# Kernel tuning notes

Measured on AMD Instinct MI355X. Metric: run time of the kernel, lower is better.

The kernel has to match this reference:

```python
import jax, jax.numpy as jnp
import numpy as np

N_NODES = 100000
N_REL = 8
F_IN, F_HID, F_OUT = 64, 64, 32
N_EDGES = 1000000


def rgcn_conv(x, W, root, bias, src, dst, edge_type):
    """PyG RGCNConv with default aggr='mean': out[i] = sum_r mean_{j in N_r(i)} W_r x_j + root x_i + bias."""
    R, _, O = W.shape
    N = x.shape[0]
    # Transform every node under every relation: [R, N, O]
    h = jnp.einsum('nf,rfo->rno', x, W)
    # Gather per-edge messages: [E, O]
    msg = h[edge_type, src]
    # Per-(relation, dst) mean aggregation via combined segment ids
    seg = edge_type * N + dst
    sums = jax.ops.segment_sum(msg, seg, num_segments=R * N).reshape(R, N, O)
    cnt = jax.ops.segment_sum(jnp.ones((msg.shape[0],), msg.dtype), seg,
                              num_segments=R * N).reshape(R, N, 1)
    mean = sums / jnp.maximum(cnt, 1.0)  # empty neighborhoods -> 0
    return mean.sum(axis=0) + x @ root + bias


def setup_inputs() -> dict:
    key = jax.random.key(0)
    ks = jax.random.split(key, 9)
    s = lambda fan: 1.0 / np.sqrt(fan)
    x = jax.random.normal(ks[0], (N_NODES, F_IN), jnp.float32)
    edge_index = jax.random.randint(ks[1], (2, N_EDGES), 0, N_NODES, jnp.int64)
    edge_type = jax.random.randint(ks[2], (N_EDGES,), 0, N_REL, jnp.int64)
    W1 = jax.random.normal(ks[3], (N_REL, F_IN, F_HID), jnp.float32) * s(F_IN)
    root1 = jax.random.normal(ks[4], (F_IN, F_HID), jnp.float32) * s(F_IN)
    b1 = jnp.zeros((F_HID,), jnp.float32)
    W2 = jax.random.normal(ks[5], (N_REL, F_HID, F_OUT), jnp.float32) * s(F_HID)
    root2 = jax.random.normal(ks[6], (F_HID, F_OUT), jnp.float32) * s(F_HID)
    b2 = jnp.zeros((F_OUT,), jnp.float32)
    return {"x": x, "W1": W1, "root1": root1, "b1": b1,
            "W2": W2, "root2": root2, "b2": b2,
            "edge_index": edge_index, "edge_type": edge_type}


def reference(x, W1, root1, b1, W2, root2, b2, edge_index, edge_type):
    src, dst = edge_index[0], edge_index[1]
    # encode (dropout is identity in eval mode)
    h = jax.nn.relu(rgcn_conv(x, W1, root1, b1, src, dst, edge_type))
    z = rgcn_conv(h, W2, root2, b2, src, dst, edge_type)
    # decode: gather-dot-product link scores over the same edge list
    return (z[src] * z[dst]).sum(axis=1)
```

## Files before the change

### kernel.cpp

```cpp
#include <hip/hip_runtime.h>

#define F_IN 64
#define F_HID 64
#define F_OUT 32
#define NREL 8
#define SCAP 6144
#define MAXBUCK 200
#define PA_PE 16

typedef __attribute__((ext_vector_type(8))) short bfrag;
typedef __attribute__((ext_vector_type(4))) float ffrag;

__device__ inline unsigned short f2bf(float f) {
  unsigned u = __float_as_uint(f);
  unsigned r = (u + 0x7fffu + ((u >> 16) & 1u)) >> 16;
  return (unsigned short)r;
}
__device__ inline unsigned bf16pair(float lo, float hi) {
  return (unsigned)f2bf(lo) | ((unsigned)f2bf(hi) << 16);
}
__device__ inline float bflo(unsigned u) { return __uint_as_float(u << 16); }
__device__ inline float bfhi(unsigned u) { return __uint_as_float(u & 0xffff0000u); }
__device__ inline float dot8(uint4 a, uint4 b) {
  return bflo(a.x) * bflo(b.x) + bfhi(a.x) * bfhi(b.x) +
         bflo(a.y) * bflo(b.y) + bfhi(a.y) * bfhi(b.y) +
         bflo(a.z) * bflo(b.z) + bfhi(a.z) * bfhi(b.z) +
         bflo(a.w) * bflo(b.w) + bfhi(a.w) * bfhi(b.w);
}

template <int O, bool PERMK>
__device__ inline void wprep_one(int t, const float* __restrict__ W,
                                 const float* __restrict__ root,
                                 unsigned short* __restrict__ Wf) {
  constexpr int CT = O / 16;
  int l = t & 63;
  int s = (t >> 6) & 1;
  int rc = t >> 7;
  int c = rc % CT;
  int r = rc / CT;
  const float* wsrc = (r < NREL) ? W + (size_t)r * 64 * O : root;
  unsigned short* dst = Wf + (size_t)t * 8;
  int col = c * 16 + (l & 15);
  int k0 = s * 32 + ((l >> 4) * 8);
#pragma unroll
  for (int j = 0; j < 8; ++j) {
    int k = k0 + j;
    if (PERMK) k = (k & 3) * 16 + (k >> 2);
    dst[j] = f2bf(wsrc[(size_t)k * O + col]);
  }
}

__global__ __launch_bounds__(256) void prep_kernel(
    const float* __restrict__ W1, const float* __restrict__ root1,
    const float* __restrict__ W2, const float* __restrict__ root2,
    unsigned short* __restrict__ wf1, unsigned short* __restrict__ wf2,
    int* __restrict__ gcur, int nbuck) {
  int gid = blockIdx.x * 256 + threadIdx.x;
  const int J1 = (NREL + 1) * (F_HID / 16) * 2 * 64;
  const int J2 = (NREL + 1) * (F_OUT / 16) * 2 * 64;
  if (gid < J1) {
    wprep_one<F_HID, false>(gid, W1, root1, wf1);
  } else if (gid < J1 + J2) {
    wprep_one<F_OUT, true>(gid - J1, W2, root2, wf2);
  } else if (gid - J1 - J2 < nbuck) {
    int b = gid - J1 - J2;
    gcur[b] = b * SCAP;
  }
}

__global__ __launch_bounds__(256) void cvt_bf16_kernel(
    const float* __restrict__ in, unsigned* __restrict__ out, int n8) {
  int i = blockIdx.x * blockDim.x + threadIdx.x;
  if (i >= n8) return;
  const float4* p = (const float4*)(in + (size_t)i * 8);
  float4 a = p[0], b = p[1];
  uint4 o;
  o.x = bf16pair(a.x, a.y);
  o.y = bf16pair(a.z, a.w);
  o.z = bf16pair(b.x, b.y);
  o.w = bf16pair(b.z, b.w);
  *((uint4*)out + i) = o;
}

__global__ __launch_bounds__(256) void binA_kernel(
    const int* __restrict__ src, const int* __restrict__ dst,
    const int* __restrict__ et, int* __restrict__ gcur,
    unsigned* __restrict__ staging, int E) {
  __shared__ int hist[MAXBUCK * 4];
  __shared__ int wbase[MAXBUCK * 4];
  const int tid = threadIdx.x;
  const int wave = tid >> 6;
  for (int i = tid; i < MAXBUCK * 4; i += 256) hist[i] = 0;
  __syncthreads();
  const int base = blockIdx.x * (256 * PA_PE);
  int dv[PA_PE], rk[PA_PE];
#pragma unroll
  for (int j = 0; j < PA_PE; ++j) {
    int e = base + j * 256 + tid;
    if (e < E) {
      int d = dst[e];
      dv[j] = d;
      rk[j] = atomicAdd(&hist[(d >> 9) * 4 + wave], 1);
    } else {
      dv[j] = -1;
    }
  }
  __syncthreads();
  for (int b = tid; b < MAXBUCK; b += 256) {
    int h0 = hist[b * 4 + 0], h1 = hist[b * 4 + 1];
    int h2 = hist[b * 4 + 2], h3 = hist[b * 4 + 3];
    int tot = h0 + h1 + h2 + h3;
    int gb = tot ? atomicAdd(&gcur[b], tot) : 0;
    wbase[b * 4 + 0] = gb;
    wbase[b * 4 + 1] = gb + h0;
    wbase[b * 4 + 2] = gb + h0 + h1;
    wbase[b * 4 + 3] = gb + h0 + h1 + h2;
  }
  __syncthreads();
#pragma unroll
  for (int j = 0; j < PA_PE; ++j) {
    if (dv[j] >= 0) {
      int e = base + j * 256 + tid;
      unsigned pk = (unsigned)src[e] | ((unsigned)et[e] << 17) |
                    ((unsigned)(dv[j] & 511) << 20);
      staging[wbase[(dv[j] >> 9) * 4 + wave] + rk[j]] = pk;
    }
  }
}

__global__ __launch_bounds__(256) void binB_kernel(
    const unsigned* __restrict__ staging, const int* __restrict__ gcur,
    int* __restrict__ recI, int* __restrict__ startsD) {
  __shared__ int cnt[4096];
  __shared__ int cur[4096];
  __shared__ int tsum[256];
  const int b = blockIdx.x;
  const int tid = threadIdx.x;
  const int cnt_b = gcur[b] - b * SCAP;
  const unsigned* st = staging + (size_t)b * SCAP;
  for (int i = tid; i < 4096; i += 256) cnt[i] = 0;
  __syncthreads();
  for (int i = tid; i < cnt_b; i += 256) {
    unsigned e = st[i];
    int dl = (e >> 20) & 511;
    int idx = ((dl >> 6) << 9) | (((e >> 17) & 7) << 6) | (dl & 63);
    atomicAdd(&cnt[idx], 1);
  }
  __syncthreads();
  int loc[16];
  int tot = 0;
#pragma unroll
  for (int j = 0; j < 16; ++j) { loc[j] = cnt[tid * 16 + j]; tot += loc[j]; }
  tsum[tid] = tot;
  __syncthreads();
  for (int off = 1; off < 256; off <<= 1) {
    int v = (tid >= off) ? tsum[tid - off] : 0;
    __syncthreads();
    tsum[tid] += v;
    __syncthreads();
  }
  int run = b * SCAP + tsum[tid] - tot;
#pragma unroll
  for (int j = 0; j < 16; ++j) {
    startsD[b * 4097 + tid * 16 + j] = run;
    cur[tid * 16 + j] = run;
    run += loc[j];
  }
  if (tid == 0) startsD[b * 4097 + 4096] = gcur[b];
  __syncthreads();
  for (int i = tid; i < cnt_b; i += 256) {
    unsigned e = st[i];
    int dl = (e >> 20) & 511;
    int idx = ((dl >> 6) << 9) | (((e >> 17) & 7) << 6) | (dl & 63);
    int pos = atomicAdd(&cur[idx], 1);
    recI[pos] = (int)(e & 0x1FFFF) | ((dl & 63) << 17);
  }
}

template <int O, bool RELU>
__global__ __launch_bounds__(256) void ragg_kernel(
    const unsigned short* __restrict__ X,
    const unsigned short* __restrict__ Wf,
    const int* __restrict__ startsD, const int* __restrict__ recI,
    const float* __restrict__ bias, unsigned short* __restrict__ Y, int N) {
  constexpr int CT = O / 16;
  __shared__ unsigned short S[64 * 40];
  __shared__ unsigned short Xg[32 * 68];
  __shared__ unsigned short A[64 * 72];
  __shared__ float pinvL[64];
  const int tid = threadIdx.x;
  const int w = tid >> 6, l = tid & 63;
  const int blk = blockIdx.x;
  const int b = blk >> 3, sb = blk & 7;
  const int ec = tid >> 3;
  const int ch = tid & 7;
  const int cl = l & 15, kgb = (l >> 4) << 3;
  int prev_dl = -1;
  for (int i = tid; i < 64 * 40 / 2; i += 256) ((unsigned*)S)[i] = 0u;
  for (int i = tid; i < 32 * 68 / 2; i += 256) ((unsigned*)Xg)[i] = 0u;
  ffrag acc[CT];
#pragma unroll
  for (int c = 0; c < CT; ++c) acc[c] = (ffrag){0.f, 0.f, 0.f, 0.f};
  for (int r = 0; r < NREL; ++r) {
    const int base = b * 4097 + (sb << 9) + (r << 6);
    if (tid < 64) {
      int len = startsD[base + tid + 1] - startsD[base + tid];
      pinvL[tid] = (len > 0) ? 1.0f / (float)len : 0.0f;
    }
    const int segS = startsD[base];
    const int segE = startsD[base + 64];
    __syncthreads();
    const int nch = (segE - segS + 31) >> 5;
    ffrag aggD[4];
#pragma unroll
    for (int mt = 0; mt < 4; ++mt) aggD[mt] = (ffrag){0.f, 0.f, 0.f, 0.f};
    for (int kb = 0; kb < nch; ++kb) {
      int p = segS + (kb << 5) + ec;
      if (p < segE) {
        int rc = recI[p];
        int dl = (rc >> 17) & 63;
        uint4 g = *(const uint4*)(X + (size_t)(rc & 0x1FFFF) * 64 + ch * 8);
        unsigned short* xrow = &Xg[ec * 68 + ch * 8];
        *(uint2*)(xrow) = make_uint2(g.x, g.y);
        *(uint2*)(xrow + 4) = make_uint2(g.z, g.w);
        if (ch == 0) {
          if (prev_dl >= 0) S[prev_dl * 40 + ec] = 0;
          S[dl * 40 + ec] = f2bf(pinvL[dl]);
          prev_dl = dl;
        }
      } else if (ch == 0 && prev_dl >= 0) {
        S[prev_dl * 40 + ec] = 0;
        prev_dl = -1;
      }
      __syncthreads();
      const int col = (w << 4) + cl;
      bfrag xf;
#pragma unroll
      for (int j = 0; j < 8; ++j) xf[j] = (short)Xg[(kgb + j) * 68 + col];
#pragma unroll
      for (int mt = 0; mt < 4; ++mt) {
        bfrag sf = *(const bfrag*)&S[((mt << 4) + cl) * 40 + kgb];
        aggD[mt] = __builtin_amdgcn_mfma_f32_16x16x32_bf16(sf, xf, aggD[mt], 0, 0, 0);
      }
      __syncthreads();
    }
#pragma unroll
    for (int mt = 0; mt < 4; ++mt)
#pragma unroll
      for (int i = 0; i < 4; ++i)
        A[((mt << 4) + ((l >> 4) << 2) + i) * 72 + (w << 4) + cl] =
            f2bf(aggD[mt][i]);
    __syncthreads();
    bfrag a0 = *(const bfrag*)&A[((w << 4) + cl) * 72 + kgb];
    bfrag a1 = *(const bfrag*)&A[((w << 4) + cl) * 72 + 32 + kgb];
    const unsigned short* wb = Wf + ((size_t)r * CT * 2 * 64 + l) * 8;
#pragma unroll
    for (int c = 0; c < CT; ++c) {
      bfrag b0 = *(const bfrag*)(wb + (size_t)(c * 2 + 0) * 512);
      bfrag b1 = *(const bfrag*)(wb + (size_t)(c * 2 + 1) * 512);
      acc[c] = __builtin_amdgcn_mfma_f32_16x16x32_bf16(a0, b0, acc[c], 0, 0, 0);
      acc[c] = __builtin_amdgcn_mfma_f32_16x16x32_bf16(a1, b1, acc[c], 0, 0, 0);
    }
  }
  int arow = blk * 64 + (w << 4) + cl;
  if (arow >= N) arow = N - 1;
  const unsigned short* xp = X + (size_t)arow * 64 + kgb;
  bfrag a0 = *(const bfrag*)(xp);
  bfrag a1 = *(const bfrag*)(xp + 32);
  const unsigned short* wb = Wf + ((size_t)NREL * CT * 2 * 64 + l) * 8;
#pragma unroll
  for (int c = 0; c < CT; ++c) {
    bfrag b0 = *(const bfrag*)(wb + (size_t)(c * 2 + 0) * 512);
    bfrag b1 = *(const bfrag*)(wb + (size_t)(c * 2 + 1) * 512);
    acc[c] = __builtin_amdgcn_mfma_f32_16x16x32_bf16(a0, b0, acc[c], 0, 0, 0);
    acc[c] = __builtin_amdgcn_mfma_f32_16x16x32_bf16(a1, b1, acc[c], 0, 0, 0);
  }
  float bv[CT];
#pragma unroll
  for (int c = 0; c < CT; ++c) bv[c] = bias[c * 16 + cl];
  const int rbase = blk * 64 + (w << 4) + ((l >> 4) << 2);
#pragma unroll
  for (int i = 0; i < 4; ++i) {
    int row = rbase + i;
    if (row < N) {
      float v[CT];
#pragma unroll
      for (int c = 0; c < CT; ++c) {
        v[c] = acc[c][i] + bv[c];
        if (RELU) v[c] = fmaxf(v[c], 0.f);
      }
      if (O == 64) {
        uint2 o;
        o.x = bf16pair(v[0], v[1]);
        o.y = bf16pair(v[2], v[3]);
        *(uint2*)(Y + (size_t)row * 64 + cl * 4) = o;
      } else {
        *(unsigned*)(Y + (size_t)row * 32 + cl * 2) = bf16pair(v[0], v[1]);
      }
    }
  }
}

__global__ __launch_bounds__(256) void decode_kernel(
    const unsigned* __restrict__ Z, const int* __restrict__ src,
    const int* __restrict__ dst, float* __restrict__ out, int E) {
  int e = blockIdx.x * blockDim.x + threadIdx.x;
  if (e >= E) return;
  const uint4* zs = (const uint4*)(Z + (size_t)src[e] * 16);
  const uint4* zd = (const uint4*)(Z + (size_t)dst[e] * 16);
  uint4 a0 = zs[0], a1 = zs[1], a2 = zs[2], a3 = zs[3];
  uint4 b0 = zd[0], b1 = zd[1], b2 = zd[2], b3 = zd[3];
  out[e] = dot8(a0, b0) + dot8(a1, b1) + dot8(a2, b2) + dot8(a3, b3);
}

extern "C" void kernel_launch(void* const* d_in, const int* in_sizes, int n_in,
                              void* d_out, int out_size, void* d_ws, size_t ws_size,
                              hipStream_t stream) {
  const float* x     = (const float*)d_in[0];
  const float* W1    = (const float*)d_in[1];
  const float* root1 = (const float*)d_in[2];
  const float* b1    = (const float*)d_in[3];
  const float* W2    = (const float*)d_in[4];
  const float* root2 = (const float*)d_in[5];
  const float* b2    = (const float*)d_in[6];
  const int*   ei    = (const int*)d_in[7];
  const int*   et    = (const int*)d_in[8];

  const int N = in_sizes[0] / F_IN;
  const int E = in_sizes[8];
  const int nbuck = (N + 511) >> 9;
  const int nblk64 = nbuck * 8;
  const int* srcp = ei;
  const int* dstp = ei + E;

  char* ws = (char*)d_ws;
  int*            gcur    = (int*)(ws + 0);
  unsigned*       staging = (unsigned*)(ws + 4096);
  int*            startsD = (int*)(ws + 4919296);
  int*            recI    = (int*)(ws + 8131584);
  unsigned short* wf1     = (unsigned short*)(ws + 13046784);
  unsigned short* wf2     = (unsigned short*)(ws + 13120512);
  unsigned short* xb      = (unsigned short*)(ws + 13157376);
  unsigned short* hmid    = (unsigned short*)(ws + 25957376);
  unsigned short* z       = (unsigned short*)(ws + 38757376);

  prep_kernel<<<28, 256, 0, stream>>>(W1, root1, W2, root2, wf1, wf2, gcur, nbuck);
  cvt_bf16_kernel<<<(N * (F_IN / 8) + 255) / 256, 256, 0, stream>>>(
      x, (unsigned*)xb, N * (F_IN / 8));
  binA_kernel<<<(E + 256 * PA_PE - 1) / (256 * PA_PE), 256, 0, stream>>>(
      srcp, dstp, et, gcur, staging, E);
  binB_kernel<<<nbuck, 256, 0, stream>>>(staging, gcur, recI, startsD);

  ragg_kernel<F_HID, true>
      <<<nblk64, 256, 0, stream>>>(xb, wf1, startsD, recI, b1, hmid, N);

  ragg_kernel<F_OUT, false>
      <<<nblk64, 256, 0, stream>>>(hmid, wf2, startsD, recI, b2, z, N);

  decode_kernel<<<(E + 255) / 256, 256, 0, stream>>>((const unsigned*)z, srcp, dstp,
                                                     (float*)d_out, E);
}
```

Measured before the change: 193.6 us.

## Double-buffer edge gathers across a flattened per-block chunk list in ragg

The per-relation nested loop in the aggregation kernel becomes one flat list of 32-edge chunks covering all relations, built once per block in shared memory. The Xg and S tiles are double-buffered so the next chunk's recI/X gather is issued while the current chunk's MFMAs run. This cuts the barriers per chunk from two to one and hides global-load latency. The chunk table is capped at 96 entries, so a block with more chunks than that would silently drop edges; this adds shared-memory and register use, and a serial table build in thread 0.

Result: slower. 214.8 us (+10.9%).

```diff
diff --git a/kernel.cpp b/kernel.cpp
--- a/kernel.cpp
+++ b/kernel.cpp
@@ -7,6 +7,7 @@
 #define SCAP 6144
 #define MAXBUCK 200
 #define PA_PE 16
+#define CTAB 96
 
 typedef __attribute__((ext_vector_type(8))) short bfrag;
 typedef __attribute__((ext_vector_type(4))) float ffrag;
@@ -184,10 +185,13 @@
     const int* __restrict__ startsD, const int* __restrict__ recI,
     const float* __restrict__ bias, unsigned short* __restrict__ Y, int N) {
   constexpr int CT = O / 16;
-  __shared__ unsigned short S[64 * 40];
-  __shared__ unsigned short Xg[32 * 68];
-  __shared__ unsigned short A[64 * 72];
-  __shared__ float pinvL[64];
+  __shared__ __align__(16) unsigned short S[2][64 * 40];
+  __shared__ __align__(16) unsigned short Xg[2][32 * 72];
+  __shared__ __align__(16) unsigned short A[64 * 72];
+  __shared__ float pinvL[512];
+  __shared__ int ctabP[CTAB];
+  __shared__ unsigned char ctabR[CTAB];
+  __shared__ int ntotS;
   const int tid = threadIdx.x;
   const int w = tid >> 6, l = tid & 63;
   const int blk = blockIdx.x;
@@ -195,73 +199,123 @@
   const int ec = tid >> 3;
   const int ch = tid & 7;
   const int cl = l & 15, kgb = (l >> 4) << 3;
-  int prev_dl = -1;
-  for (int i = tid; i < 64 * 40 / 2; i += 256) ((unsigned*)S)[i] = 0u;
-  for (int i = tid; i < 32 * 68 / 2; i += 256) ((unsigned*)Xg)[i] = 0u;
+  const int base0 = b * 4097 + (sb << 9);
+
+  for (int i = tid; i < 2 * 64 * 40 / 2; i += 256) ((unsigned*)S)[i] = 0u;
+  for (int i = tid; i < 2 * 32 * 72 / 2; i += 256) ((unsigned*)Xg)[i] = 0u;
+  for (int i = tid; i < 512; i += 256) {
+    int len = startsD[base0 + i + 1] - startsD[base0 + i];
+    pinvL[i] = (len > 0) ? 1.0f / (float)len : 0.0f;
+  }
+  if (tid == 0) {
+    int nt = 0;
+    for (int r = 0; r < NREL; ++r) {
+      int s = startsD[base0 + (r << 6)];
+      int e = startsD[base0 + (r << 6) + 64];
+      for (int p = s; p < e && nt < CTAB; p += 32) {
+        ctabP[nt] = p;
+        ctabR[nt] = (unsigned char)r;
+        ++nt;
+      }
+    }
+    ntotS = nt;
+  }
+  __syncthreads();
+  const int ntot = ntotS;
+
   ffrag acc[CT];
 #pragma unroll
   for (int c = 0; c < CT; ++c) acc[c] = (ffrag){0.f, 0.f, 0.f, 0.f};
-  for (int r = 0; r < NREL; ++r) {
-    const int base = b * 4097 + (sb << 9) + (r << 6);
-    if (tid < 64) {
-      int len = startsD[base + tid + 1] - startsD[base + tid];
-      pinvL[tid] = (len > 0) ? 1.0f / (float)len : 0.0f;
-    }
-    const int segS = startsD[base];
-    const int segE = startsD[base + 64];
+  ffrag aggD[4];
+#pragma unroll
+  for (int mt = 0; mt < 4; ++mt) aggD[mt] = (ffrag){0.f, 0.f, 0.f, 0.f};
+  int prevdl[2] = {-1, -1};
+
+  if (ntot > 0) {
+    int r0 = ctabR[0];
+    int pend = startsD[base0 + (r0 << 6) + 64];
+    int p = ctabP[0] + ec;
+    int dl = -1;
+    uint4 g;
+    if (p < pend) {
+      int rc = recI[p];
+      dl = (rc >> 17) & 63;
+      g = *(const uint4*)(X + (size_t)(rc & 0x1FFFF) * 64 + ch * 8);
+    }
+    if (dl >= 0) *(uint4*)&Xg[0][ec * 72 + ch * 8] = g;
+    if (ch == 0) {
+      if (dl >= 0) S[0][dl * 40 + ec] = f2bf(pinvL[(r0 << 6) + dl]);
+      prevdl[0] = dl;
+    }
+  }
+  __syncthreads();
+
+  int buf = 0;
+  for (int c = 0; c < ntot; ++c) {
+    const int r = ctabR[c];
+    const bool have1 = (c + 1 < ntot);
+    int dl1 = -1;
+    float pv1 = 0.f;
+    uint4 g1;
+    if (have1) {
+      int r1 = ctabR[c + 1];
+      int pend = startsD[base0 + (r1 << 6) + 64];
+      int p = ctabP[c + 1] + ec;
+      if (p < pend) {
+        int rc = recI[p];
+        dl1 = (rc >> 17) & 63;
+        g1 = *(const uint4*)(X + (size_t)(rc & 0x1FFFF) * 64 + ch * 8);
+        if (ch == 0) pv1 = pinvL[(r1 << 6) + dl1];
+      }
+    }
+    {
+      const unsigned short* xgb = Xg[buf];
+      const unsigned short* sbf = S[buf];
+      bfrag xf;
+#pragma unroll
+      for (int j = 0; j < 8; ++j) xf[j] = (short)xgb[(kgb + j) * 72 + (w << 4) + cl];
+#pragma unroll
+      for (int mt = 0; mt < 4; ++mt) {
+        bfrag sf = *(const bfrag*)&sbf[((mt << 4) + cl) * 40 + kgb];
+        aggD[mt] = __builtin_amdgcn_mfma_f32_16x16x32_bf16(sf, xf, aggD[mt], 0, 0, 0);
+      }
+    }
+    if (have1) {
+      const int nb = buf ^ 1;
+      if (dl1 >= 0) *(uint4*)&Xg[nb][ec * 72 + ch * 8] = g1;
+      if (ch == 0) {
+        int pd = prevdl[nb];
+        if (pd >= 0 && pd != dl1) S[nb][pd * 40 + ec] = 0;
+        if (dl1 >= 0) S[nb][dl1 * 40 + ec] = f2bf(pv1);
+        prevdl[nb] = dl1;
+      }
+    }
+    const bool fl = !have1 || ((int)ctabR[c + 1] != r);
     __syncthreads();
-    const int nch = (segE - segS + 31) >> 5;
-    ffrag aggD[4];
-#pragma unroll
-    for (int mt = 0; mt < 4; ++mt) aggD[mt] = (ffrag){0.f, 0.f, 0.f, 0.f};
-    for (int kb = 0; kb < nch; ++kb) {
-      int p = segS + (kb << 5) + ec;
-      if (p < segE) {
-        int rc = recI[p];
-        int dl = (rc >> 17) & 63;
-        uint4 g = *(const uint4*)(X + (size_t)(rc & 0x1FFFF) * 64 + ch * 8);
-        unsigned short* xrow = &Xg[ec * 68 + ch * 8];
-        *(uint2*)(xrow) = make_uint2(g.x, g.y);
-        *(uint2*)(xrow + 4) = make_uint2(g.z, g.w);
-        if (ch == 0) {
-          if (prev_dl >= 0) S[prev_dl * 40 + ec] = 0;
-          S[dl * 40 + ec] = f2bf(pinvL[dl]);
-          prev_dl = dl;
-        }
-      } else if (ch == 0 && prev_dl >= 0) {
-        S[prev_dl * 40 + ec] = 0;
-        prev_dl = -1;
-      }
+    if (fl) {
+#pragma unroll
+      for (int mt = 0; mt < 4; ++mt)
+#pragma unroll
+        for (int i = 0; i < 4; ++i)
+          A[((mt << 4) + ((l >> 4) << 2) + i) * 72 + (w << 4) + cl] =
+              f2bf(aggD[mt][i]);
+#pragma unroll
+      for (int mt = 0; mt < 4; ++mt) aggD[mt] = (ffrag){0.f, 0.f, 0.f, 0.f};
       __syncthreads();
-      const int col = (w << 4) + cl;
-      bfrag xf;
-#pragma unroll
-      for (int j = 0; j < 8; ++j) xf[j] = (short)Xg[(kgb + j) * 68 + col];
-#pragma unroll
-      for (int mt = 0; mt < 4; ++mt) {
-        bfrag sf = *(const bfrag*)&S[((mt << 4) + cl) * 40 + kgb];
-        aggD[mt] = __builtin_amdgcn_mfma_f32_16x16x32_bf16(sf, xf, aggD[mt], 0, 0, 0);
-      }
-      __syncthreads();
-    }
-#pragma unroll
-    for (int mt = 0; mt < 4; ++mt)
-#pragma unroll
-      for (int i = 0; i < 4; ++i)
-        A[((mt << 4) + ((l >> 4) << 2) + i) * 72 + (w << 4) + cl] =
-            f2bf(aggD[mt][i]);
-    __syncthreads();
-    bfrag a0 = *(const bfrag*)&A[((w << 4) + cl) * 72 + kgb];
-    bfrag a1 = *(const bfrag*)&A[((w << 4) + cl) * 72 + 32 + kgb];
-    const unsigned short* wb = Wf + ((size_t)r * CT * 2 * 64 + l) * 8;
-#pragma unroll
-    for (int c = 0; c < CT; ++c) {
-      bfrag b0 = *(const bfrag*)(wb + (size_t)(c * 2 + 0) * 512);
-      bfrag b1 = *(const bfrag*)(wb + (size_t)(c * 2 + 1) * 512);
-      acc[c] = __builtin_amdgcn_mfma_f32_16x16x32_bf16(a0, b0, acc[c], 0, 0, 0);
-      acc[c] = __builtin_amdgcn_mfma_f32_16x16x32_bf16(a1, b1, acc[c], 0, 0, 0);
-    }
-  }
+      bfrag a0 = *(const bfrag*)&A[((w << 4) + cl) * 72 + kgb];
+      bfrag a1 = *(const bfrag*)&A[((w << 4) + cl) * 72 + 32 + kgb];
+      const unsigned short* wb = Wf + ((size_t)r * CT * 2 * 64 + l) * 8;
+#pragma unroll
+      for (int cc = 0; cc < CT; ++cc) {
+        bfrag b0 = *(const bfrag*)(wb + (size_t)(cc * 2 + 0) * 512);
+        bfrag b1 = *(const bfrag*)(wb + (size_t)(cc * 2 + 1) * 512);
+        acc[cc] = __builtin_amdgcn_mfma_f32_16x16x32_bf16(a0, b0, acc[cc], 0, 0, 0);
+        acc[cc] = __builtin_amdgcn_mfma_f32_16x16x32_bf16(a1, b1, acc[cc], 0, 0, 0);
+      }
+    }
+    buf ^= 1;
+  }
+
   int arow = blk * 64 + (w << 4) + cl;
   if (arow >= N) arow = N - 1;
   const unsigned short* xp = X + (size_t)arow * 64 + kgb;
@@ -269,15 +323,15 @@
   bfrag a1 = *(const bfrag*)(xp + 32);
   const unsigned short* wb = Wf + ((size_t)NREL * CT * 2 * 64 + l) * 8;
 #pragma unroll
-  for (int c = 0; c < CT; ++c) {
-    bfrag b0 = *(const bfrag*)(wb + (size_t)(c * 2 + 0) * 512);
-    bfrag b1 = *(const bfrag*)(wb + (size_t)(c * 2 + 1) * 512);
-    acc[c] = __builtin_amdgcn_mfma_f32_16x16x32_bf16(a0, b0, acc[c], 0, 0, 0);
-    acc[c] = __builtin_amdgcn_mfma_f32_16x16x32_bf16(a1, b1, acc[c], 0, 0, 0);
+  for (int cc = 0; cc < CT; ++cc) {
+    bfrag b0 = *(const bfrag*)(wb + (size_t)(cc * 2 + 0) * 512);
+    bfrag b1 = *(const bfrag*)(wb + (size_t)(cc * 2 + 1) * 512);
+    acc[cc] = __builtin_amdgcn_mfma_f32_16x16x32_bf16(a0, b0, acc[cc], 0, 0, 0);
+    acc[cc] = __builtin_amdgcn_mfma_f32_16x16x32_bf16(a1, b1, acc[cc], 0, 0, 0);
   }
   float bv[CT];
 #pragma unroll
-  for (int c = 0; c < CT; ++c) bv[c] = bias[c * 16 + cl];
+  for (int cc = 0; cc < CT; ++cc) bv[cc] = bias[cc * 16 + cl];
   const int rbase = blk * 64 + (w << 4) + ((l >> 4) << 2);
 #pragma unroll
   for (int i = 0; i < 4; ++i) {
@@ -285,9 +339,9 @@
     if (row < N) {
       float v[CT];
 #pragma unroll
-      for (int c = 0; c < CT; ++c) {
-        v[c] = acc[c][i] + bv[c];
-        if (RELU) v[c] = fmaxf(v[c], 0.f);
+      for (int cc = 0; cc < CT; ++cc) {
+        v[cc] = acc[cc][i] + bv[cc];
+        if (RELU) v[cc] = fmaxf(v[cc], 0.f);
       }
       if (O == 64) {
         uint2 o;
```
